# Performance work log

Hardware: AMD Instinct MI355X
Metric: run time of the kernel (lower is better)

Reference implementation:

```python
import jax, jax.numpy as jnp
import numpy as np

N_NODES = 50000
N_EDGES = 400000
NUM_FEATS = 128
LATENT_DIM_Y = 64
HIDDEN = 512
OUT = 2


def gcn_conv(x, edge_index, W, b, num_nodes):
    """PyG GCNConv: add self-loops, symmetric normalization, x @ W then scatter-add."""
    x = x @ W  # [N, out_ch]
    loop = jnp.arange(num_nodes)
    row = jnp.concatenate([edge_index[0], loop])  # source nodes
    col = jnp.concatenate([edge_index[1], loop])  # target nodes
    deg = jax.ops.segment_sum(jnp.ones_like(col, dtype=x.dtype), col, num_segments=num_nodes)
    dinv = jnp.where(deg > 0, jax.lax.rsqrt(deg), 0.0)
    norm = dinv[row] * dinv[col]  # [E+N]
    msgs = norm[:, None] * x[row]  # gather source features, scale
    out = jax.ops.segment_sum(msgs, col, num_segments=num_nodes)
    return out + b


def setup_inputs() -> dict:
    key = jax.random.key(0)
    k1, k2, k3, k4, k5, k6, k7 = jax.random.split(key, 7)
    in_ch = NUM_FEATS + LATENT_DIM_Y
    inputs = {
        "edge_index": jax.random.randint(k1, (2, N_EDGES), 0, N_NODES),
        "X": jax.random.normal(k2, (N_NODES, NUM_FEATS), dtype=jnp.float32),
        "u_Y": jax.random.normal(k3, (N_NODES, LATENT_DIM_Y), dtype=jnp.float32),
        "W1": jax.random.normal(k4, (in_ch, HIDDEN), dtype=jnp.float32) / np.sqrt(in_ch),
        "b1": jnp.zeros((HIDDEN,), dtype=jnp.float32),
        "W2": jax.random.normal(k5, (HIDDEN, OUT), dtype=jnp.float32) / np.sqrt(HIDDEN),
        "b2": jnp.zeros((OUT,), dtype=jnp.float32),
    }
    return inputs


def reference(edge_index, X, u_Y, W1, b1, W2, b2):
    latent = jnp.concatenate([u_Y, X], axis=1)  # [N, latent+feats]
    h = jax.nn.relu(gcn_conv(latent, edge_index, W1, b1, N_NODES))
    y = gcn_conv(h, edge_index, W2, b2, N_NODES)
    # nn.Softmax() on a 2D tensor defaults to dim=1
    return jax.nn.softmax(y, axis=1)
```

## Files before the change

kernel.cpp:

```cpp
#include <hip/hip_runtime.h>

#define N_NODES 50000
#define N_EDGES 400000
#define FEATS   128
#define LAT     64
#define IN_CH   192
#define HID     512
#define MB      64
#define NB      196

typedef __attribute__((ext_vector_type(8))) short bf16x8;
typedef __attribute__((ext_vector_type(4))) float f32x4;

static inline int cdiv(int a, int b) { return (a + b - 1) / b; }

__device__ __forceinline__ unsigned short f2bf(float f) {
    unsigned int u = __float_as_uint(f);
    u = (u + 0x7fffu + ((u >> 16) & 1u)) >> 16;
    return (unsigned short)u;
}
__device__ __forceinline__ float bf_lo(unsigned int u) {
    return __uint_as_float(u << 16);
}
__device__ __forceinline__ float bf_hi(unsigned int u) {
    return __uint_as_float(u & 0xffff0000u);
}


__global__ void k_count(const int* __restrict__ col, int* __restrict__ cnt) {
    int e = blockIdx.x * blockDim.x + threadIdx.x;
    if (e < N_EDGES) atomicAdd(&cnt[col[e]], 1);
}

__global__ __launch_bounds__(256) void
k_block_reduce(const int* __restrict__ cnt, int* __restrict__ bsum) {
    __shared__ int wsums[4];
    int i = blockIdx.x * 256 + threadIdx.x;
    int v = (i < N_NODES) ? cnt[i] : 0;
#pragma unroll
    for (int off = 32; off; off >>= 1) v += __shfl_down(v, off);
    if ((threadIdx.x & 63) == 0) wsums[threadIdx.x >> 6] = v;
    __syncthreads();
    if (threadIdx.x == 0) bsum[blockIdx.x] = wsums[0] + wsums[1] + wsums[2] + wsums[3];
}

__global__ __launch_bounds__(256) void
k_scan_bsums(const int* __restrict__ bsum, int* __restrict__ bex) {
    __shared__ int wsums[4];
    int t = threadIdx.x, lane = t & 63, wid = t >> 6;
    int v = (t < NB) ? bsum[t] : 0;
    int x = v;
#pragma unroll
    for (int off = 1; off < 64; off <<= 1) {
        int y = __shfl_up(x, off);
        if (lane >= off) x += y;
    }
    if (lane == 63) wsums[wid] = x;
    __syncthreads();
    int wo = 0;
    for (int w = 0; w < wid; ++w) wo += wsums[w];
    if (t < NB) bex[t] = wo + x - v;
}

__global__ __launch_bounds__(256) void
k_block_scan(const int* __restrict__ cnt, const int* __restrict__ bex,
             int* __restrict__ row_start, int* __restrict__ cursor,
             float* __restrict__ dinv) {
    __shared__ int wsums[4];
    int t = threadIdx.x, lane = t & 63, wid = t >> 6;
    int i = blockIdx.x * 256 + t;
    int v = (i < N_NODES) ? cnt[i] : 0;
    int x = v;
#pragma unroll
    for (int off = 1; off < 64; off <<= 1) {
        int y = __shfl_up(x, off);
        if (lane >= off) x += y;
    }
    if (lane == 63) wsums[wid] = x;
    __syncthreads();
    int wo = 0;
    for (int w = 0; w < wid; ++w) wo += wsums[w];
    int ex = bex[blockIdx.x] + wo + x - v;
    if (i < N_NODES) {
        row_start[i] = ex;
        cursor[i]    = ex;
        dinv[i]      = rsqrtf((float)(v + 1));
    }
    if (blockIdx.x == 0 && t == 0) row_start[N_NODES] = N_EDGES;
}

__global__ void k_scatter(const int* __restrict__ ei, int* __restrict__ cursor,
                          int* __restrict__ csr_src) {
    int e = blockIdx.x * blockDim.x + threadIdx.x;
    if (e >= N_EDGES) return;
    int r = ei[e];
    int c = ei[N_EDGES + e];
    int pos = atomicAdd(&cursor[c], 1);
    csr_src[pos] = r;
}

__global__ void k_cvt_latent(const float* __restrict__ uY, const float* __restrict__ X,
                             unsigned short* __restrict__ latent) {
    int idx = blockIdx.x * blockDim.x + threadIdx.x;
    if (idx >= N_NODES * 48) return;
    int i = idx / 48, q = idx % 48;
    const float4* uY4 = (const float4*)uY;
    const float4* X4  = (const float4*)X;
    float4 v = (q < LAT / 4) ? uY4[i * (LAT / 4) + q]
                             : X4[i * (FEATS / 4) + (q - LAT / 4)];
    uint2 o;
    o.x = (unsigned int)f2bf(v.x) | ((unsigned int)f2bf(v.y) << 16);
    o.y = (unsigned int)f2bf(v.z) | ((unsigned int)f2bf(v.w) << 16);
    ((uint2*)latent)[idx] = o;
}

__global__ void k_w1_tile(const float* __restrict__ W1, unsigned short* __restrict__ W1f) {
    int idx = blockIdx.x * blockDim.x + threadIdx.x;
    if (idx >= IN_CH * HID) return;
    int k = idx / HID, n = idx % HID;
    int ntile = n >> 4, nn = n & 15;
    int kc = k >> 5, q = (k >> 3) & 3, j = k & 7;
    int dst = (((ntile * 6 + kc) * 64 + q * 16 + nn) << 3) + j;
    W1f[dst] = f2bf(W1[idx]);
}

__global__ __launch_bounds__(256) void
k_gather_agg(const int* __restrict__ row_start, const int* __restrict__ csr_src,
             const float* __restrict__ dinv,
             const unsigned short* __restrict__ latent, unsigned short* __restrict__ agg) {
    int w    = blockIdx.x * 4 + (threadIdx.x >> 6);
    int lane = threadIdx.x & 63;
    if (w >= N_NODES) return;
    int half = lane >> 5, l = lane & 31;
    int l3 = l * 3;
    const unsigned int* __restrict__ L = (const unsigned int*)latent;

    float di = dinv[w];
    float acc0 = 0.f, acc1 = 0.f, acc2 = 0.f, acc3 = 0.f, acc4 = 0.f, acc5 = 0.f;
    if (half == 0) {
        const unsigned int* p = L + w * 96 + l3;
        unsigned int u0 = p[0], u1 = p[1], u2 = p[2];
        acc0 = di * bf_lo(u0); acc1 = di * bf_hi(u0);
        acc2 = di * bf_lo(u1); acc3 = di * bf_hi(u1);
        acc4 = di * bf_lo(u2); acc5 = di * bf_hi(u2);
    }

    int jlo = row_start[w], jhi = row_start[w + 1];
    int j = jlo + half;
    int r = (j < jhi) ? csr_src[j] : 0;
    for (; j < jhi; j += 2) {
        int rn = (j + 2 < jhi) ? csr_src[j + 2] : 0;
        float wt = dinv[r];
        const unsigned int* p = L + r * 96 + l3;
        unsigned int u0 = p[0], u1 = p[1], u2 = p[2];
        acc0 = fmaf(wt, bf_lo(u0), acc0);
        acc1 = fmaf(wt, bf_hi(u0), acc1);
        acc2 = fmaf(wt, bf_lo(u1), acc2);
        acc3 = fmaf(wt, bf_hi(u1), acc3);
        acc4 = fmaf(wt, bf_lo(u2), acc4);
        acc5 = fmaf(wt, bf_hi(u2), acc5);
        r = rn;
    }

    acc0 += __shfl_xor(acc0, 32);
    acc1 += __shfl_xor(acc1, 32);
    acc2 += __shfl_xor(acc2, 32);
    acc3 += __shfl_xor(acc3, 32);
    acc4 += __shfl_xor(acc4, 32);
    acc5 += __shfl_xor(acc5, 32);

    if (half == 0) {
        unsigned int* q = (unsigned int*)agg + w * 96 + l3;
        q[0] = (unsigned int)f2bf(di * acc0) | ((unsigned int)f2bf(di * acc1) << 16);
        q[1] = (unsigned int)f2bf(di * acc2) | ((unsigned int)f2bf(di * acc3) << 16);
        q[2] = (unsigned int)f2bf(di * acc4) | ((unsigned int)f2bf(di * acc5) << 16);
    }
}

__global__ __launch_bounds__(256, 2) void
k_gemm_mfma(const unsigned short* __restrict__ agg, const unsigned short* __restrict__ W1f,
            const float* __restrict__ b1, const float* __restrict__ W2,
            float* __restrict__ y_pre) {
    __shared__ unsigned short Af[MB * IN_CH];
    __shared__ float red[4][MB][2];

    int t  = threadIdx.x;
    int m0 = blockIdx.x * MB;

    {
        const uint4* src = (const uint4*)agg;
        for (int idx = t; idx < MB * 24; idx += 256) {
            int row = idx / 24, c = idx % 24;
            int g = m0 + row;
            uint4 v = make_uint4(0u, 0u, 0u, 0u);
            if (g < N_NODES) v = src[(size_t)g * 24 + c];
            int mt = row >> 4, m = row & 15, kc = c >> 2, q = c & 3;
            ((uint4*)Af)[(mt * 6 + kc) * 64 + q * 16 + m] = v;
        }
    }
    __syncthreads();

    int wid = t >> 6, lane = t & 63;
    int nl = lane & 15, q = lane >> 4;

    float b1v[8], w2a[8], w2b[8];
#pragma unroll
    for (int nt = 0; nt < 8; ++nt) {
        int n = wid * 128 + nt * 16 + nl;
        b1v[nt] = b1[n];
        w2a[nt] = W2[n * 2 + 0];
        w2b[nt] = W2[n * 2 + 1];
    }

    f32x4 acc[4][8];
#pragma unroll
    for (int mt = 0; mt < 4; ++mt)
#pragma unroll
        for (int nt = 0; nt < 8; ++nt) acc[mt][nt] = (f32x4){0.f, 0.f, 0.f, 0.f};

    const bf16x8* Afv = (const bf16x8*)Af;
    const bf16x8* Bv  = (const bf16x8*)W1f;
#pragma unroll
    for (int kc = 0; kc < 6; ++kc) {
        bf16x8 a[4];
#pragma unroll
        for (int mt = 0; mt < 4; ++mt) a[mt] = Afv[(mt * 6 + kc) * 64 + lane];
#pragma unroll
        for (int nt = 0; nt < 8; ++nt) {
            bf16x8 b = Bv[((wid * 8 + nt) * 6 + kc) * 64 + lane];
#pragma unroll
            for (int mt = 0; mt < 4; ++mt)
                acc[mt][nt] = __builtin_amdgcn_mfma_f32_16x16x32_bf16(a[mt], b, acc[mt][nt], 0, 0, 0);
        }
    }

#pragma unroll
    for (int mt = 0; mt < 4; ++mt) {
#pragma unroll
        for (int r = 0; r < 4; ++r) {
            float p0 = 0.f, p1 = 0.f;
#pragma unroll
            for (int nt = 0; nt < 8; ++nt) {
                float h = fmaxf(acc[mt][nt][r] + b1v[nt], 0.f);
                p0 = fmaf(h, w2a[nt], p0);
                p1 = fmaf(h, w2b[nt], p1);
            }
#pragma unroll
            for (int off = 1; off < 16; off <<= 1) {
                p0 += __shfl_xor(p0, off);
                p1 += __shfl_xor(p1, off);
            }
            if (nl == 0) {
                int row = mt * 16 + q * 4 + r;
                red[wid][row][0] = p0;
                red[wid][row][1] = p1;
            }
        }
    }
    __syncthreads();
    if (t < MB * 2) {
        int row = t >> 1, j = t & 1;
        float s = red[0][row][j] + red[1][row][j] + red[2][row][j] + red[3][row][j];
        int g = m0 + row;
        if (g < N_NODES) y_pre[g * 2 + j] = s;
    }
}

__global__ void k_gather_y(const int* __restrict__ row_start, const int* __restrict__ csr_src,
                           const float* __restrict__ dinv,
                           const float* __restrict__ y_pre, const float* __restrict__ b2,
                           float* __restrict__ out) {
    int i = blockIdx.x * blockDim.x + threadIdx.x;
    if (i >= N_NODES) return;
    float di = dinv[i];
    float a0 = di * y_pre[i * 2 + 0];
    float a1 = di * y_pre[i * 2 + 1];
    int jlo = row_start[i], jhi = row_start[i + 1];
    for (int j = jlo; j < jhi; ++j) {
        int   r  = csr_src[j];
        float wt = dinv[r];
        a0 = fmaf(wt, y_pre[r * 2 + 0], a0);
        a1 = fmaf(wt, y_pre[r * 2 + 1], a1);
    }
    float ya = di * a0 + b2[0];
    float yb = di * a1 + b2[1];
    float mx = fmaxf(ya, yb);
    float e0 = expf(ya - mx);
    float e1 = expf(yb - mx);
    float inv = 1.0f / (e0 + e1);
    out[i * 2 + 0] = e0 * inv;
    out[i * 2 + 1] = e1 * inv;
}


extern "C" void kernel_launch(void* const* d_in, const int* in_sizes, int n_in,
                              void* d_out, int out_size, void* d_ws, size_t ws_size,
                              hipStream_t stream) {
    const int*   ei = (const int*)d_in[0];
    const float* X  = (const float*)d_in[1];
    const float* uY = (const float*)d_in[2];
    const float* W1 = (const float*)d_in[3];
    const float* b1 = (const float*)d_in[4];
    const float* W2 = (const float*)d_in[5];
    const float* b2 = (const float*)d_in[6];
    float* out = (float*)d_out;

    char* ws = (char*)d_ws;
    auto carve = [&](size_t bytes) {
        char* p = ws;
        ws += (bytes + 255) & ~size_t(255);
        return p;
    };
    int*   cnt       = (int*)carve(N_NODES * sizeof(int));
    int*   bsum      = (int*)carve(NB * sizeof(int));
    int*   bex       = (int*)carve(NB * sizeof(int));
    int*   row_start = (int*)carve((N_NODES + 1) * sizeof(int));
    int*   cursor    = (int*)carve(N_NODES * sizeof(int));
    int*   csr_src   = (int*)carve((size_t)N_EDGES * sizeof(int));
    float* dinv      = (float*)carve(N_NODES * sizeof(float));
    unsigned short* latent = (unsigned short*)carve((size_t)N_NODES * IN_CH * 2);
    unsigned short* aggb   = (unsigned short*)carve((size_t)N_NODES * IN_CH * 2);
    unsigned short* W1f    = (unsigned short*)carve((size_t)IN_CH * HID * 2);
    float* y_pre     = (float*)carve((size_t)N_NODES * 2 * sizeof(float));

    hipMemsetAsync(cnt, 0, N_NODES * sizeof(int), stream);
    k_count       <<<cdiv(N_EDGES, 256), 256, 0, stream>>>(ei + N_EDGES, cnt);
    k_block_reduce<<<NB, 256, 0, stream>>>(cnt, bsum);
    k_scan_bsums  <<<1, 256, 0, stream>>>(bsum, bex);
    k_block_scan  <<<NB, 256, 0, stream>>>(cnt, bex, row_start, cursor, dinv);
    k_scatter     <<<cdiv(N_EDGES, 256), 256, 0, stream>>>(ei, cursor, csr_src);

    k_cvt_latent  <<<cdiv(N_NODES * 48, 256), 256, 0, stream>>>(uY, X, latent);
    k_w1_tile     <<<cdiv(IN_CH * HID, 256), 256, 0, stream>>>(W1, W1f);

    k_gather_agg  <<<cdiv(N_NODES, 4), 256, 0, stream>>>(row_start, csr_src, dinv, latent, aggb);

    k_gemm_mfma   <<<cdiv(N_NODES, MB), 256, 0, stream>>>(aggb, W1f, b1, W2, y_pre);

    k_gather_y    <<<cdiv(N_NODES, 256), 256, 0, stream>>>(row_start, csr_src, dinv, y_pre, b2, out);
}
```

Before: 211.8 us.

## Merge prep kernels into one launch and widen per-node gather parallelism

The edge-count, latent bf16 conversion and W1 retiling kernels are merged into a single block-partitioned launch, which cuts launch overhead and lets the independent work overlap. The layer-1 gather now spreads each node's edges across four 16-lane groups with 12 accumulators per lane instead of two 32-lane halves. The layer-2 gather uses 8 lanes per node with a shuffle reduction instead of one thread per node, which aims to fix load imbalance and improve memory parallelism. The cost is more register pressure and extra shuffle reductions.

```diff
diff --git a/kernel.cpp b/kernel.cpp
--- a/kernel.cpp
+++ b/kernel.cpp
@@ -9,6 +9,10 @@
 #define MB      64
 #define NB      196
 
+#define CNT_BLKS 1563
+#define CVT_BLKS 9375
+#define W1_BLKS  384
+
 typedef __attribute__((ext_vector_type(8))) short bf16x8;
 typedef __attribute__((ext_vector_type(4))) float f32x4;
 
@@ -26,10 +30,36 @@
     return __uint_as_float(u & 0xffff0000u);
 }
 
-
-__global__ void k_count(const int* __restrict__ col, int* __restrict__ cnt) {
-    int e = blockIdx.x * blockDim.x + threadIdx.x;
-    if (e < N_EDGES) atomicAdd(&cnt[col[e]], 1);
+__global__ __launch_bounds__(256) void
+k_front(const int* __restrict__ col, int* __restrict__ cnt,
+        const float* __restrict__ uY, const float* __restrict__ X,
+        unsigned short* __restrict__ latent,
+        const float* __restrict__ W1, unsigned short* __restrict__ W1f) {
+    int bid = blockIdx.x;
+    if (bid < CNT_BLKS) {
+        int e = bid * 256 + threadIdx.x;
+        if (e < N_EDGES) atomicAdd(&cnt[col[e]], 1);
+    } else if (bid < CNT_BLKS + CVT_BLKS) {
+        int idx = (bid - CNT_BLKS) * 256 + threadIdx.x;
+        int i = idx / 48, q = idx % 48;
+        const float4* uY4 = (const float4*)uY;
+        const float4* X4  = (const float4*)X;
+        float4 v = (q < LAT / 4) ? uY4[i * (LAT / 4) + q]
+                                 : X4[i * (FEATS / 4) + (q - LAT / 4)];
+        uint2 o;
+        o.x = (unsigned int)f2bf(v.x) | ((unsigned int)f2bf(v.y) << 16);
+        o.y = (unsigned int)f2bf(v.z) | ((unsigned int)f2bf(v.w) << 16);
+        ((uint2*)latent)[idx] = o;
+    } else {
+        int idx = (bid - CNT_BLKS - CVT_BLKS) * 256 + threadIdx.x;
+        if (idx < IN_CH * HID) {
+            int k = idx / HID, n = idx % HID;
+            int ntile = n >> 4, nn = n & 15;
+            int kc = k >> 5, q = (k >> 3) & 3, j = k & 7;
+            int dst = (((ntile * 6 + kc) * 64 + q * 16 + nn) << 3) + j;
+            W1f[dst] = f2bf(W1[idx]);
+        }
+    }
 }
 
 __global__ __launch_bounds__(256) void
@@ -99,31 +129,6 @@
     csr_src[pos] = r;
 }
 
-__global__ void k_cvt_latent(const float* __restrict__ uY, const float* __restrict__ X,
-                             unsigned short* __restrict__ latent) {
-    int idx = blockIdx.x * blockDim.x + threadIdx.x;
-    if (idx >= N_NODES * 48) return;
-    int i = idx / 48, q = idx % 48;
-    const float4* uY4 = (const float4*)uY;
-    const float4* X4  = (const float4*)X;
-    float4 v = (q < LAT / 4) ? uY4[i * (LAT / 4) + q]
-                             : X4[i * (FEATS / 4) + (q - LAT / 4)];
-    uint2 o;
-    o.x = (unsigned int)f2bf(v.x) | ((unsigned int)f2bf(v.y) << 16);
-    o.y = (unsigned int)f2bf(v.z) | ((unsigned int)f2bf(v.w) << 16);
-    ((uint2*)latent)[idx] = o;
-}
-
-__global__ void k_w1_tile(const float* __restrict__ W1, unsigned short* __restrict__ W1f) {
-    int idx = blockIdx.x * blockDim.x + threadIdx.x;
-    if (idx >= IN_CH * HID) return;
-    int k = idx / HID, n = idx % HID;
-    int ntile = n >> 4, nn = n & 15;
-    int kc = k >> 5, q = (k >> 3) & 3, j = k & 7;
-    int dst = (((ntile * 6 + kc) * 64 + q * 16 + nn) << 3) + j;
-    W1f[dst] = f2bf(W1[idx]);
-}
-
 __global__ __launch_bounds__(256) void
 k_gather_agg(const int* __restrict__ row_start, const int* __restrict__ csr_src,
              const float* __restrict__ dinv,
@@ -131,49 +136,60 @@
     int w    = blockIdx.x * 4 + (threadIdx.x >> 6);
     int lane = threadIdx.x & 63;
     if (w >= N_NODES) return;
-    int half = lane >> 5, l = lane & 31;
-    int l3 = l * 3;
+    int qt = lane >> 4, l = lane & 15;
+    int c0 = l * 6;
     const unsigned int* __restrict__ L = (const unsigned int*)latent;
 
     float di = dinv[w];
-    float acc0 = 0.f, acc1 = 0.f, acc2 = 0.f, acc3 = 0.f, acc4 = 0.f, acc5 = 0.f;
-    if (half == 0) {
-        const unsigned int* p = L + w * 96 + l3;
-        unsigned int u0 = p[0], u1 = p[1], u2 = p[2];
-        acc0 = di * bf_lo(u0); acc1 = di * bf_hi(u0);
-        acc2 = di * bf_lo(u1); acc3 = di * bf_hi(u1);
-        acc4 = di * bf_lo(u2); acc5 = di * bf_hi(u2);
+    float acc[12];
+    if (qt == 0) {
+        const unsigned int* p = L + w * 96 + c0;
+#pragma unroll
+        for (int d = 0; d < 6; ++d) {
+            unsigned int u = p[d];
+            acc[2 * d]     = di * bf_lo(u);
+            acc[2 * d + 1] = di * bf_hi(u);
+        }
+    } else {
+#pragma unroll
+        for (int d = 0; d < 12; ++d) acc[d] = 0.f;
     }
 
     int jlo = row_start[w], jhi = row_start[w + 1];
-    int j = jlo + half;
+    int j = jlo + qt;
     int r = (j < jhi) ? csr_src[j] : 0;
-    for (; j < jhi; j += 2) {
-        int rn = (j + 2 < jhi) ? csr_src[j + 2] : 0;
+    for (; j < jhi; j += 4) {
+        int rn = (j + 4 < jhi) ? csr_src[j + 4] : 0;
         float wt = dinv[r];
-        const unsigned int* p = L + r * 96 + l3;
-        unsigned int u0 = p[0], u1 = p[1], u2 = p[2];
-        acc0 = fmaf(wt, bf_lo(u0), acc0);
-        acc1 = fmaf(wt, bf_hi(u0), acc1);
-        acc2 = fmaf(wt, bf_lo(u1), acc2);
-        acc3 = fmaf(wt, bf_hi(u1), acc3);
-        acc4 = fmaf(wt, bf_lo(u2), acc4);
-        acc5 = fmaf(wt, bf_hi(u2), acc5);
+        const unsigned int* p = L + r * 96 + c0;
+        unsigned int u0 = p[0], u1 = p[1], u2 = p[2], u3 = p[3], u4 = p[4], u5 = p[5];
+        acc[0]  = fmaf(wt, bf_lo(u0), acc[0]);
+        acc[1]  = fmaf(wt, bf_hi(u0), acc[1]);
+        acc[2]  = fmaf(wt, bf_lo(u1), acc[2]);
+        acc[3]  = fmaf(wt, bf_hi(u1), acc[3]);
+        acc[4]  = fmaf(wt, bf_lo(u2), acc[4]);
+        acc[5]  = fmaf(wt, bf_hi(u2), acc[5]);
+        acc[6]  = fmaf(wt, bf_lo(u3), acc[6]);
+        acc[7]  = fmaf(wt, bf_hi(u3), acc[7]);
+        acc[8]  = fmaf(wt, bf_lo(u4), acc[8]);
+        acc[9]  = fmaf(wt, bf_hi(u4), acc[9]);
+        acc[10] = fmaf(wt, bf_lo(u5), acc[10]);
+        acc[11] = fmaf(wt, bf_hi(u5), acc[11]);
         r = rn;
     }
 
-    acc0 += __shfl_xor(acc0, 32);
-    acc1 += __shfl_xor(acc1, 32);
-    acc2 += __shfl_xor(acc2, 32);
-    acc3 += __shfl_xor(acc3, 32);
-    acc4 += __shfl_xor(acc4, 32);
-    acc5 += __shfl_xor(acc5, 32);
-
-    if (half == 0) {
-        unsigned int* q = (unsigned int*)agg + w * 96 + l3;
-        q[0] = (unsigned int)f2bf(di * acc0) | ((unsigned int)f2bf(di * acc1) << 16);
-        q[1] = (unsigned int)f2bf(di * acc2) | ((unsigned int)f2bf(di * acc3) << 16);
-        q[2] = (unsigned int)f2bf(di * acc4) | ((unsigned int)f2bf(di * acc5) << 16);
+#pragma unroll
+    for (int d = 0; d < 12; ++d) {
+        acc[d] += __shfl_xor(acc[d], 16);
+        acc[d] += __shfl_xor(acc[d], 32);
+    }
+
+    if (qt == 0) {
+        unsigned int* qp = (unsigned int*)agg + w * 96 + c0;
+#pragma unroll
+        for (int d = 0; d < 6; ++d)
+            qp[d] = (unsigned int)f2bf(di * acc[2 * d]) |
+                    ((unsigned int)f2bf(di * acc[2 * d + 1]) << 16);
     }
 }
 
@@ -266,30 +282,42 @@
     }
 }
 
-__global__ void k_gather_y(const int* __restrict__ row_start, const int* __restrict__ csr_src,
-                           const float* __restrict__ dinv,
-                           const float* __restrict__ y_pre, const float* __restrict__ b2,
-                           float* __restrict__ out) {
-    int i = blockIdx.x * blockDim.x + threadIdx.x;
+__global__ __launch_bounds__(256) void
+k_gather_y(const int* __restrict__ row_start, const int* __restrict__ csr_src,
+           const float* __restrict__ dinv,
+           const float* __restrict__ y_pre, const float* __restrict__ b2,
+           float* __restrict__ out) {
+    int i  = blockIdx.x * 32 + (threadIdx.x >> 3);
+    int l8 = threadIdx.x & 7;
     if (i >= N_NODES) return;
     float di = dinv[i];
-    float a0 = di * y_pre[i * 2 + 0];
-    float a1 = di * y_pre[i * 2 + 1];
+    float a0 = 0.f, a1 = 0.f;
+    if (l8 == 0) {
+        a0 = di * y_pre[i * 2 + 0];
+        a1 = di * y_pre[i * 2 + 1];
+    }
     int jlo = row_start[i], jhi = row_start[i + 1];
-    for (int j = jlo; j < jhi; ++j) {
+    for (int j = jlo + l8; j < jhi; j += 8) {
         int   r  = csr_src[j];
         float wt = dinv[r];
         a0 = fmaf(wt, y_pre[r * 2 + 0], a0);
         a1 = fmaf(wt, y_pre[r * 2 + 1], a1);
     }
-    float ya = di * a0 + b2[0];
-    float yb = di * a1 + b2[1];
-    float mx = fmaxf(ya, yb);
-    float e0 = expf(ya - mx);
-    float e1 = expf(yb - mx);
-    float inv = 1.0f / (e0 + e1);
-    out[i * 2 + 0] = e0 * inv;
-    out[i * 2 + 1] = e1 * inv;
+#pragma unroll
+    for (int off = 1; off < 8; off <<= 1) {
+        a0 += __shfl_xor(a0, off);
+        a1 += __shfl_xor(a1, off);
+    }
+    if (l8 == 0) {
+        float ya = di * a0 + b2[0];
+        float yb = di * a1 + b2[1];
+        float mx = fmaxf(ya, yb);
+        float e0 = expf(ya - mx);
+        float e1 = expf(yb - mx);
+        float inv = 1.0f / (e0 + e1);
+        out[i * 2 + 0] = e0 * inv;
+        out[i * 2 + 1] = e1 * inv;
+    }
 }
 
 
@@ -324,18 +352,16 @@
     float* y_pre     = (float*)carve((size_t)N_NODES * 2 * sizeof(float));
 
     hipMemsetAsync(cnt, 0, N_NODES * sizeof(int), stream);
-    k_count       <<<cdiv(N_EDGES, 256), 256, 0, stream>>>(ei + N_EDGES, cnt);
+    k_front       <<<CNT_BLKS + CVT_BLKS + W1_BLKS, 256, 0, stream>>>(
+                        ei + N_EDGES, cnt, uY, X, latent, W1, W1f);
     k_block_reduce<<<NB, 256, 0, stream>>>(cnt, bsum);
     k_scan_bsums  <<<1, 256, 0, stream>>>(bsum, bex);
     k_block_scan  <<<NB, 256, 0, stream>>>(cnt, bex, row_start, cursor, dinv);
     k_scatter     <<<cdiv(N_EDGES, 256), 256, 0, stream>>>(ei, cursor, csr_src);
 
-    k_cvt_latent  <<<cdiv(N_NODES * 48, 256), 256, 0, stream>>>(uY, X, latent);
-    k_w1_tile     <<<cdiv(IN_CH * HID, 256), 256, 0, stream>>>(W1, W1f);
-
     k_gather_agg  <<<cdiv(N_NODES, 4), 256, 0, stream>>>(row_start, csr_src, dinv, latent, aggb);
 
     k_gemm_mfma   <<<cdiv(N_NODES, MB), 256, 0, stream>>>(aggb, W1f, b1, W2, y_pre);
 
-    k_gather_y    <<<cdiv(N_NODES, 256), 256, 0, stream>>>(row_start, csr_src, dinv, y_pre, b2, out);
-}
+    k_gather_y    <<<cdiv(N_NODES, 32), 256, 0, stream>>>(row_start, csr_src, dinv, y_pre, b2, out);
+}
```

After: 202.5 us. -4.4%, faster.
